# Kernel optimization log

Measured on AMD Instinct MI355X. Metric: run time of the kernel, lower is better.

## Reference

```python
import jax, jax.numpy as jnp
import numpy as np


def setup_inputs() -> dict:
    key = jax.random.key(0)
    k1, k2, k3 = jax.random.split(key, 3)
    B, C, S, D = 8, 256, 2048, 64
    a = jax.random.normal(k1, (B, C, S), dtype=jnp.float32)
    b = jax.random.normal(k2, (B, S, D), dtype=jnp.float32)
    c = jax.random.normal(k3, (B, S, D), dtype=jnp.float32)
    return {"a": a, "b": b, "c": c}


def reference(a, b, c):
    # mid[b, n, m] = softmax_m(b @ c^T), unscaled
    scores = jnp.einsum("bnd,bmd->bnm", b, c)
    mid = jax.nn.softmax(scores, axis=-1)  # [B, S, S]
    # out = a @ mid^T + a  -> [B, C, S]
    out = jnp.einsum("bcm,bnm->bcn", a, mid) + a
    return out
```

## Files before the change

kernel.cpp:

```cpp
#include <hip/hip_runtime.h>
#include <stdint.h>

#define S 2048
#define DHEAD 64
#define CDIM 256
#define NBATCH 8
#define NMT 16
#define NSTEP 32

typedef __attribute__((ext_vector_type(4))) float f32x4;
typedef __attribute__((ext_vector_type(8))) short s16x8;
typedef __attribute__((ext_vector_type(8))) _Float16 f16x8;
typedef __attribute__((ext_vector_type(4))) unsigned short u16x4;

static __device__ __forceinline__ unsigned short f2bf(float f) {
    unsigned int u = __builtin_bit_cast(unsigned int, f);
    unsigned int r = (u + 0x7FFFu + ((u >> 16) & 1u)) >> 16;
    return (unsigned short)r;
}
static __device__ __forceinline__ unsigned short f2h(float f) {
    _Float16 h = (_Float16)f;
    return __builtin_bit_cast(unsigned short, h);
}
static __device__ __forceinline__ float bf2f(unsigned short u) {
    return __builtin_bit_cast(float, (unsigned int)u << 16);
}

#define GLOAD16(g, l)                                                              \
    __builtin_amdgcn_global_load_lds(                                              \
        (const __attribute__((address_space(1))) void*)(g),                        \
        (__attribute__((address_space(3))) void*)(l), 16, 0, 0)

__global__ __launch_bounds__(256) void cvt_kernel(
    const float* __restrict__ a, const float* __restrict__ b, const float* __restrict__ c,
    unsigned short* __restrict__ a16, unsigned short* __restrict__ b16,
    unsigned short* __restrict__ c16)
{
    const int na4 = NBATCH * CDIM * S / 4;
    const int nbc4 = NBATCH * S * DHEAD / 4;
    int i0 = blockIdx.x * 256 + threadIdx.x;
    int stride = gridDim.x * 256;
    for (int i = i0; i < na4; i += stride) {
        f32x4 v = ((const f32x4*)a)[i];
        u16x4 o; o.x = f2bf(v.x); o.y = f2bf(v.y); o.z = f2bf(v.z); o.w = f2bf(v.w);
        ((u16x4*)a16)[i] = o;
    }
    for (int i = i0; i < nbc4; i += stride) {
        f32x4 v = ((const f32x4*)b)[i];
        u16x4 o; o.x = f2h(v.x); o.y = f2h(v.y); o.z = f2h(v.z); o.w = f2h(v.w);
        ((u16x4*)b16)[i] = o;
        f32x4 u = ((const f32x4*)c)[i];
        u16x4 p; p.x = f2h(u.x); p.y = f2h(u.y); p.z = f2h(u.z); p.w = f2h(u.w);
        ((u16x4*)c16)[i] = p;
    }
}

__global__ __launch_bounds__(256) void scores_kernel(
    const unsigned short* __restrict__ B16, const unsigned short* __restrict__ C16,
    unsigned short* __restrict__ E, float* __restrict__ Lp, int b0, int nb)
{
    const int bid = blockIdx.x;
    int lb, idx;
    if (nb == 8) { lb = bid & 7; idx = bid >> 3; }
    else { lb = bid / (NMT * 16); idx = bid - lb * (NMT * 16); }
    const int gb = b0 + lb;
    const int mt = idx & 15;
    const int m0 = mt * 128;
    const int n0 = (idx >> 4) * 128;
    const unsigned short* __restrict__ bp = B16 + (size_t)gb * S * DHEAD;
    const unsigned short* __restrict__ cp = C16 + (size_t)gb * S * DHEAD;
    unsigned short* __restrict__ Ep = E + (size_t)lb * S * S;

    extern __shared__ char smem[];
    unsigned short* cs = (unsigned short*)smem;
    unsigned short* bs = cs + 128 * 64;
    unsigned short* es = (unsigned short*)smem;
    float* Lsh = (float*)(smem + 34816);

    const int tid = threadIdx.x;
    const int lane = tid & 63;
    const int w = tid >> 6;
    const int wr = w >> 1, wc = w & 1;
    const int q = lane >> 4, r15 = lane & 15;

    #pragma unroll
    for (int t = 0; t < 4; ++t) {
        int r = w + 4 * t;
        int ch = r * 64 + lane;
        int row = ch >> 3;
        int off = ((ch & 7) ^ (row & 7)) * 8;
        GLOAD16(cp + (size_t)(m0 + row) * DHEAD + off, &cs[r * 512]);
        GLOAD16(bp + (size_t)(n0 + row) * DHEAD + off, &bs[r * 512]);
    }
    __syncthreads();

    f32x4 acc[4][4] = {};
    #pragma unroll
    for (int kk = 0; kk < 2; ++kk) {
        const int sz = ((kk * 4 + q) ^ (r15 & 7)) * 8;
        f16x8 af[4], bf[4];
        #pragma unroll
        for (int i = 0; i < 4; ++i)
            af[i] = *(const f16x8*)&cs[(wr * 64 + i * 16 + r15) * 64 + sz];
        #pragma unroll
        for (int j = 0; j < 4; ++j)
            bf[j] = *(const f16x8*)&bs[(wc * 64 + j * 16 + r15) * 64 + sz];
        #pragma unroll
        for (int i = 0; i < 4; ++i)
            #pragma unroll
            for (int j = 0; j < 4; ++j)
                acc[i][j] = __builtin_amdgcn_mfma_f32_16x16x32_f16(af[i], bf[j], acc[i][j], 0, 0, 0);
    }

    u16x4 pk[4][4];
    float sj[4] = {0.f, 0.f, 0.f, 0.f};
    #pragma unroll
    for (int i = 0; i < 4; ++i) {
        #pragma unroll
        for (int j = 0; j < 4; ++j) {
            float e0 = __expf(acc[i][j][0]);
            float e1 = __expf(acc[i][j][1]);
            float e2 = __expf(acc[i][j][2]);
            float e3 = __expf(acc[i][j][3]);
            pk[i][j].x = f2bf(e0); pk[i][j].y = f2bf(e1);
            pk[i][j].z = f2bf(e2); pk[i][j].w = f2bf(e3);
            sj[j] += (e0 + e1) + (e2 + e3);
        }
    }
    #pragma unroll
    for (int j = 0; j < 4; ++j) {
        sj[j] += __shfl_xor(sj[j], 16);
        sj[j] += __shfl_xor(sj[j], 32);
    }

    __syncthreads();

    #pragma unroll
    for (int i = 0; i < 4; ++i)
        #pragma unroll
        for (int j = 0; j < 4; ++j) {
            int nl = wc * 64 + j * 16 + r15;
            int ml = wr * 64 + i * 16 + q * 4;
            *(u16x4*)&es[nl * 136 + ml] = pk[i][j];
        }
    if (q == 0) {
        #pragma unroll
        for (int j = 0; j < 4; ++j)
            Lsh[wr * 128 + wc * 64 + j * 16 + r15] = sj[j];
    }
    __syncthreads();

    if (tid < 128)
        Lp[(size_t)lb * NMT * S + (size_t)mt * S + n0 + tid] = Lsh[tid] + Lsh[128 + tid];

    #pragma unroll
    for (int t = 0; t < 8; ++t) {
        int ch = tid + 256 * t;
        int row = ch >> 4, off = ch & 15;
        f32x4 v = *(const f32x4*)&es[row * 136 + off * 8];
        *(f32x4*)&Ep[(size_t)(n0 + row) * S + m0 + off * 8] = v;
    }
}

#define GEMM_DECODE()                                                             \
    const int tid = threadIdx.x;                                                  \
    const int lane = tid & 63;                                                    \
    const int w = tid >> 6;                                                       \
    const int wr = w >> 1, wc = w & 1;                                            \
    const int q = lane >> 4, r15 = lane & 15;                                     \
    int aRow[4], aOff[4], aR_[4], bRow[2], bOff[2], bR_[2];                       \
    _Pragma("unroll")                                                             \
    for (int t = 0; t < 4; ++t) {                                                 \
        int r = w + 4 * t, ch = r * 64 + lane;                                    \
        aR_[t] = r; aRow[t] = ch >> 3;                                            \
        aOff[t] = ((ch & 7) ^ ((ch >> 3) & 7)) * 8;                               \
    }                                                                             \
    _Pragma("unroll")                                                             \
    for (int t = 0; t < 2; ++t) {                                                 \
        int r = w + 4 * t, ch = r * 64 + lane;                                    \
        bR_[t] = r; bRow[t] = ch >> 3;                                            \
        bOff[t] = ((ch & 7) ^ ((ch >> 3) & 7)) * 8;                               \
    }

#define STAGEP(bufA, bufB, k0)                                                    \
    {                                                                             \
        _Pragma("unroll")                                                         \
        for (int t = 0; t < 4; ++t)                                               \
            GLOAD16(Ap + (size_t)(c0 + aRow[t]) * S + (k0) + aOff[t],             \
                    (bufA) + aR_[t] * 512);                                       \
        _Pragma("unroll")                                                         \
        for (int t = 0; t < 2; ++t)                                               \
            GLOAD16(Bp + (size_t)(n0 + bRow[t]) * S + (k0) + bOff[t],             \
                    (bufB) + bR_[t] * 512);                                       \
    }

#define GEMM_EPILOGUE()                                                           \
    float rcpL[2];                                                                \
    _Pragma("unroll")                                                             \
    for (int j = 0; j < 2; ++j) {                                                 \
        int n = n0 + wc * 32 + j * 16 + r15;                                      \
        float s = 0.f;                                                            \
        _Pragma("unroll")                                                         \
        for (int mt = 0; mt < NMT; ++mt)                                          \
            s += Lp[(size_t)lb * NMT * S + (size_t)mt * S + n];                   \
        rcpL[j] = 1.0f / s;                                                       \
    }                                                                             \
    _Pragma("unroll")                                                             \
    for (int i = 0; i < 4; ++i) {                                                 \
        _Pragma("unroll")                                                         \
        for (int rr = 0; rr < 4; ++rr) {                                          \
            int cc = c0 + wr * 64 + i * 16 + q * 4 + rr;                          \
            size_t base = (size_t)cc * S;                                         \
            _Pragma("unroll")                                                     \
            for (int j = 0; j < 2; ++j) {                                         \
                int n = n0 + wc * 32 + j * 16 + r15;                              \
                op[base + n] = acc[i][j][rr] * rcpL[j] + bf2f(Ap[base + n]);      \
            }                                                                     \
        }                                                                         \
    }

__global__ __launch_bounds__(256, 2) void gemm_kernel3(
    const unsigned short* __restrict__ a16, const unsigned short* __restrict__ E,
    const float* __restrict__ Lp, float* __restrict__ out, int b0, int nb)
{
    const int bid = blockIdx.x;
    int lb, idx;
    if (nb == 8) { lb = bid & 7; idx = bid >> 3; }
    else { lb = bid / 64; idx = bid - lb * 64; }
    const int gb = b0 + lb;
    const int nt = idx >> 1, ct = idx & 1;
    const int n0 = nt * 64, c0 = ct * 128;

    const unsigned short* __restrict__ Ap = a16 + (size_t)gb * CDIM * S;
    const unsigned short* __restrict__ Bp = E + (size_t)lb * S * S;
    float* __restrict__ op = out + (size_t)gb * CDIM * S;

    extern __shared__ char gsm[];
    unsigned short* As[3];
    unsigned short* Bs[3];
    #pragma unroll
    for (int u = 0; u < 3; ++u) {
        As[u] = (unsigned short*)gsm + u * (128 * 64 + 64 * 64);
        Bs[u] = As[u] + 128 * 64;
    }

    GEMM_DECODE();

    f32x4 acc[4][2] = {};

    STAGEP(As[0], Bs[0], 0);
    STAGEP(As[1], Bs[1], 64);

    const int sw0 = (q ^ (r15 & 7)) * 8;
    const int sw1 = ((4 + q) ^ (r15 & 7)) * 8;

    #pragma unroll
    for (int kt = 0; kt < NSTEP; ++kt) {
        const int cur = kt % 3;
        if (kt <= NSTEP - 3) {
            STAGEP(As[(kt + 2) % 3], Bs[(kt + 2) % 3], (kt + 2) * 64);
            asm volatile("s_waitcnt vmcnt(12)" ::: "memory");
        } else if (kt == NSTEP - 2) {
            asm volatile("s_waitcnt vmcnt(6)" ::: "memory");
        } else {
            asm volatile("s_waitcnt vmcnt(0)" ::: "memory");
        }
        __builtin_amdgcn_sched_barrier(0);
        __builtin_amdgcn_s_barrier();
        __builtin_amdgcn_sched_barrier(0);

        const unsigned short* Ar = As[cur];
        const unsigned short* Br = Bs[cur];
        #pragma unroll
        for (int kk = 0; kk < 2; ++kk) {
            const int sz = kk ? sw1 : sw0;
            s16x8 af[4], bf[2];
            #pragma unroll
            for (int i = 0; i < 4; ++i)
                af[i] = *(const s16x8*)&Ar[(wr * 64 + i * 16 + r15) * 64 + sz];
            #pragma unroll
            for (int j = 0; j < 2; ++j)
                bf[j] = *(const s16x8*)&Br[(wc * 32 + j * 16 + r15) * 64 + sz];
            __builtin_amdgcn_s_setprio(1);
            #pragma unroll
            for (int i = 0; i < 4; ++i)
                #pragma unroll
                for (int j = 0; j < 2; ++j)
                    acc[i][j] = __builtin_amdgcn_mfma_f32_16x16x32_bf16(af[i], bf[j], acc[i][j], 0, 0, 0);
            __builtin_amdgcn_s_setprio(0);
        }

        __builtin_amdgcn_sched_barrier(0);
        __builtin_amdgcn_s_barrier();
    }

    GEMM_EPILOGUE();
}

__global__ __launch_bounds__(256, 2) void gemm_kernel2(
    const unsigned short* __restrict__ a16, const unsigned short* __restrict__ E,
    const float* __restrict__ Lp, float* __restrict__ out, int b0, int nb)
{
    const int bid = blockIdx.x;
    int lb, idx;
    if (nb == 8) { lb = bid & 7; idx = bid >> 3; }
    else { lb = bid / 64; idx = bid - lb * 64; }
    const int gb = b0 + lb;
    const int nt = idx >> 1, ct = idx & 1;
    const int n0 = nt * 64, c0 = ct * 128;

    const unsigned short* __restrict__ Ap = a16 + (size_t)gb * CDIM * S;
    const unsigned short* __restrict__ Bp = E + (size_t)lb * S * S;
    float* __restrict__ op = out + (size_t)gb * CDIM * S;

    __shared__ unsigned short AsS[2][128 * 64];
    __shared__ unsigned short BsS[2][64 * 64];

    GEMM_DECODE();

    f32x4 acc[4][2] = {};

    STAGEP(AsS[0], BsS[0], 0);
    __syncthreads();

    const int sw0 = (q ^ (r15 & 7)) * 8;
    const int sw1 = ((4 + q) ^ (r15 & 7)) * 8;

    #pragma unroll 2
    for (int kt = 0; kt < NSTEP; ++kt) {
        const int cur = kt & 1;
        if (kt < NSTEP - 1) STAGEP(AsS[cur ^ 1], BsS[cur ^ 1], (kt + 1) * 64);

        #pragma unroll
        for (int kk = 0; kk < 2; ++kk) {
            const int sz = kk ? sw1 : sw0;
            s16x8 af[4], bf[2];
            #pragma unroll
            for (int i = 0; i < 4; ++i)
                af[i] = *(const s16x8*)&AsS[cur][(wr * 64 + i * 16 + r15) * 64 + sz];
            #pragma unroll
            for (int j = 0; j < 2; ++j)
                bf[j] = *(const s16x8*)&BsS[cur][(wc * 32 + j * 16 + r15) * 64 + sz];
            #pragma unroll
            for (int i = 0; i < 4; ++i)
                #pragma unroll
                for (int j = 0; j < 2; ++j)
                    acc[i][j] = __builtin_amdgcn_mfma_f32_16x16x32_bf16(af[i], bf[j], acc[i][j], 0, 0, 0);
        }
        __syncthreads();
    }

    GEMM_EPILOGUE();
}

extern "C" void kernel_launch(void* const* d_in, const int* in_sizes, int n_in,
                              void* d_out, int out_size, void* d_ws, size_t ws_size,
                              hipStream_t stream) {
    const float* a = (const float*)d_in[0];
    const float* b = (const float*)d_in[1];
    const float* c = (const float*)d_in[2];
    float* out = (float*)d_out;

    const size_t a16_bytes = (size_t)NBATCH * CDIM * S * 2;
    const size_t bc_bytes = (size_t)NBATCH * S * DHEAD * 2;
    const size_t head = a16_bytes + 2 * bc_bytes;
    const size_t perb = (size_t)S * S * 2 + (size_t)NMT * S * 4;
    int G = 1;
    if (ws_size > head + perb) {
        size_t g = (ws_size - head) / perb;
        G = (g >= NBATCH) ? NBATCH : (int)g;
        if (G < 1) G = 1;
    }
    unsigned short* a16 = (unsigned short*)d_ws;
    unsigned short* b16 = (unsigned short*)((char*)d_ws + a16_bytes);
    unsigned short* c16 = (unsigned short*)((char*)d_ws + a16_bytes + bc_bytes);
    unsigned short* E = (unsigned short*)((char*)d_ws + head);
    float* Lp = (float*)((char*)d_ws + head + (size_t)G * S * S * 2);

    const int gemm_lds3 = 3 * (128 * 64 + 64 * 64) * 2;
    hipError_t attr_ok = hipFuncSetAttribute(
        reinterpret_cast<const void*>(gemm_kernel3),
        hipFuncAttributeMaxDynamicSharedMemorySize, gemm_lds3);

    cvt_kernel<<<1024, 256, 0, stream>>>(a, b, c, a16, b16, c16);

    const size_t lds1 = 34816 + 2 * 128 * 4;
    for (int b0 = 0; b0 < NBATCH; b0 += G) {
        int nb = (NBATCH - b0 < G) ? (NBATCH - b0) : G;
        scores_kernel<<<NMT * 16 * nb, 256, lds1, stream>>>(b16, c16, E, Lp, b0, nb);
        if (attr_ok == hipSuccess)
            gemm_kernel3<<<64 * nb, 256, gemm_lds3, stream>>>(a16, E, Lp, out, b0, nb);
        else
            gemm_kernel2<<<64 * nb, 256, 0, stream>>>(a16, E, Lp, out, b0, nb);
    }
}
```

Before: 50.62 us.

## Make scores kernel loop over m-tiles with double-buffered C loads

```diff
diff --git a/kernel.cpp b/kernel.cpp
--- a/kernel.cpp
+++ b/kernel.cpp
@@ -5,8 +5,8 @@
 #define DHEAD 64
 #define CDIM 256
 #define NBATCH 8
-#define NMT 16
 #define NSTEP 32
+#define SMT 8
 
 typedef __attribute__((ext_vector_type(4))) float f32x4;
 typedef __attribute__((ext_vector_type(8))) short s16x8;
@@ -55,27 +55,27 @@
     }
 }
 
-__global__ __launch_bounds__(256) void scores_kernel(
+__global__ __launch_bounds__(256, 2) void scores_kernel(
     const unsigned short* __restrict__ B16, const unsigned short* __restrict__ C16,
     unsigned short* __restrict__ E, float* __restrict__ Lp, int b0, int nb)
 {
     const int bid = blockIdx.x;
     int lb, idx;
     if (nb == 8) { lb = bid & 7; idx = bid >> 3; }
-    else { lb = bid / (NMT * 16); idx = bid - lb * (NMT * 16); }
+    else { lb = bid / 64; idx = bid - lb * 64; }
     const int gb = b0 + lb;
-    const int mt = idx & 15;
-    const int m0 = mt * 128;
-    const int n0 = (idx >> 4) * 128;
+    const int nt = idx >> 1, mh = idx & 1;
+    const int n0 = nt * 64;
+    const int mbase = mh * (SMT * 128);
+
     const unsigned short* __restrict__ bp = B16 + (size_t)gb * S * DHEAD;
     const unsigned short* __restrict__ cp = C16 + (size_t)gb * S * DHEAD;
     unsigned short* __restrict__ Ep = E + (size_t)lb * S * S;
 
-    extern __shared__ char smem[];
-    unsigned short* cs = (unsigned short*)smem;
-    unsigned short* bs = cs + 128 * 64;
-    unsigned short* es = (unsigned short*)smem;
-    float* Lsh = (float*)(smem + 34816);
+    __shared__ unsigned short bs[64 * 64];
+    __shared__ unsigned short cs[2][128 * 64];
+    __shared__ unsigned short es[64 * 136];
+    __shared__ float Lsh[4 * 32];
 
     const int tid = threadIdx.x;
     const int lane = tid & 63;
@@ -83,82 +83,118 @@
     const int wr = w >> 1, wc = w & 1;
     const int q = lane >> 4, r15 = lane & 15;
 
+    int cRow[4], cOff[4], cR_[4], bRow[2], bOff[2], bR_[2];
     #pragma unroll
     for (int t = 0; t < 4; ++t) {
-        int r = w + 4 * t;
-        int ch = r * 64 + lane;
-        int row = ch >> 3;
-        int off = ((ch & 7) ^ (row & 7)) * 8;
-        GLOAD16(cp + (size_t)(m0 + row) * DHEAD + off, &cs[r * 512]);
-        GLOAD16(bp + (size_t)(n0 + row) * DHEAD + off, &bs[r * 512]);
-    }
-    __syncthreads();
-
-    f32x4 acc[4][4] = {};
-    #pragma unroll
-    for (int kk = 0; kk < 2; ++kk) {
-        const int sz = ((kk * 4 + q) ^ (r15 & 7)) * 8;
-        f16x8 af[4], bf[4];
+        int r = w + 4 * t, ch = r * 64 + lane;
+        cR_[t] = r; cRow[t] = ch >> 3;
+        cOff[t] = ((ch & 7) ^ ((ch >> 3) & 7)) * 8;
+    }
+    #pragma unroll
+    for (int t = 0; t < 2; ++t) {
+        int r = w + 4 * t, ch = r * 64 + lane;
+        bR_[t] = r; bRow[t] = ch >> 3;
+        bOff[t] = ((ch & 7) ^ ((ch >> 3) & 7)) * 8;
+    }
+
+#define SSTAGE_C(buf, m0)                                                          \
+    {                                                                              \
+        _Pragma("unroll")                                                          \
+        for (int t = 0; t < 4; ++t)                                                \
+            GLOAD16(cp + (size_t)((m0) + cRow[t]) * DHEAD + cOff[t],               \
+                    &cs[buf][cR_[t] * 512]);                                       \
+    }
+
+    #pragma unroll
+    for (int t = 0; t < 2; ++t)
+        GLOAD16(bp + (size_t)(n0 + bRow[t]) * DHEAD + bOff[t], &bs[bR_[t] * 512]);
+    SSTAGE_C(0, mbase);
+
+    float sj[2] = {0.f, 0.f};
+
+    #pragma unroll
+    for (int mt = 0; mt < SMT; ++mt) {
+        const int cur = mt & 1;
+        const int m0 = mbase + mt * 128;
+        if (mt < SMT - 1) {
+            SSTAGE_C(cur ^ 1, m0 + 128);
+            asm volatile("s_waitcnt vmcnt(4)" ::: "memory");
+        } else {
+            asm volatile("s_waitcnt vmcnt(0)" ::: "memory");
+        }
+        __builtin_amdgcn_sched_barrier(0);
+        __builtin_amdgcn_s_barrier();
+        __builtin_amdgcn_sched_barrier(0);
+
+        f32x4 acc[4][2] = {};
+        #pragma unroll
+        for (int kk = 0; kk < 2; ++kk) {
+            const int sz = ((kk * 4 + q) ^ (r15 & 7)) * 8;
+            f16x8 af[4], bf[2];
+            #pragma unroll
+            for (int i = 0; i < 4; ++i)
+                af[i] = *(const f16x8*)&cs[cur][(wr * 64 + i * 16 + r15) * 64 + sz];
+            #pragma unroll
+            for (int j = 0; j < 2; ++j)
+                bf[j] = *(const f16x8*)&bs[(wc * 32 + j * 16 + r15) * 64 + sz];
+            __builtin_amdgcn_s_setprio(1);
+            #pragma unroll
+            for (int i = 0; i < 4; ++i)
+                #pragma unroll
+                for (int j = 0; j < 2; ++j)
+                    acc[i][j] = __builtin_amdgcn_mfma_f32_16x16x32_f16(af[i], bf[j], acc[i][j], 0, 0, 0);
+            __builtin_amdgcn_s_setprio(0);
+        }
+
+        u16x4 pk[4][2];
         #pragma unroll
         for (int i = 0; i < 4; ++i)
-            af[i] = *(const f16x8*)&cs[(wr * 64 + i * 16 + r15) * 64 + sz];
-        #pragma unroll
-        for (int j = 0; j < 4; ++j)
-            bf[j] = *(const f16x8*)&bs[(wc * 64 + j * 16 + r15) * 64 + sz];
+            #pragma unroll
+            for (int j = 0; j < 2; ++j) {
+                float e0 = __expf(acc[i][j][0]);
+                float e1 = __expf(acc[i][j][1]);
+                float e2 = __expf(acc[i][j][2]);
+                float e3 = __expf(acc[i][j][3]);
+                sj[j] += (e0 + e1) + (e2 + e3);
+                pk[i][j].x = f2bf(e0); pk[i][j].y = f2bf(e1);
+                pk[i][j].z = f2bf(e2); pk[i][j].w = f2bf(e3);
+            }
+
+        __syncthreads();
         #pragma unroll
         for (int i = 0; i < 4; ++i)
             #pragma unroll
-            for (int j = 0; j < 4; ++j)
-                acc[i][j] = __builtin_amdgcn_mfma_f32_16x16x32_f16(af[i], bf[j], acc[i][j], 0, 0, 0);
-    }
-
-    u16x4 pk[4][4];
-    float sj[4] = {0.f, 0.f, 0.f, 0.f};
-    #pragma unroll
-    for (int i = 0; i < 4; ++i) {
-        #pragma unroll
-        for (int j = 0; j < 4; ++j) {
-            float e0 = __expf(acc[i][j][0]);
-            float e1 = __expf(acc[i][j][1]);
-            float e2 = __expf(acc[i][j][2]);
-            float e3 = __expf(acc[i][j][3]);
-            pk[i][j].x = f2bf(e0); pk[i][j].y = f2bf(e1);
-            pk[i][j].z = f2bf(e2); pk[i][j].w = f2bf(e3);
-            sj[j] += (e0 + e1) + (e2 + e3);
-        }
-    }
-    #pragma unroll
-    for (int j = 0; j < 4; ++j) {
+            for (int j = 0; j < 2; ++j) {
+                int nl = wc * 32 + j * 16 + r15;
+                int ml = wr * 64 + i * 16 + q * 4;
+                *(u16x4*)&es[nl * 136 + ml] = pk[i][j];
+            }
+        __syncthreads();
+
+        #pragma unroll
+        for (int t = 0; t < 4; ++t) {
+            int ch = tid + 256 * t;
+            int row = ch >> 4, off = ch & 15;
+            f32x4 v = *(const f32x4*)&es[row * 136 + off * 8];
+            *(f32x4*)&Ep[(size_t)(n0 + row) * S + m0 + off * 8] = v;
+        }
+    }
+#undef SSTAGE_C
+
+    #pragma unroll
+    for (int j = 0; j < 2; ++j) {
         sj[j] += __shfl_xor(sj[j], 16);
         sj[j] += __shfl_xor(sj[j], 32);
     }
-
+    if (lane < 16) {
+        Lsh[w * 32 + r15] = sj[0];
+        Lsh[w * 32 + 16 + r15] = sj[1];
+    }
     __syncthreads();
-
-    #pragma unroll
-    for (int i = 0; i < 4; ++i)
-        #pragma unroll
-        for (int j = 0; j < 4; ++j) {
-            int nl = wc * 64 + j * 16 + r15;
-            int ml = wr * 64 + i * 16 + q * 4;
-            *(u16x4*)&es[nl * 136 + ml] = pk[i][j];
-        }
-    if (q == 0) {
-        #pragma unroll
-        for (int j = 0; j < 4; ++j)
-            Lsh[wr * 128 + wc * 64 + j * 16 + r15] = sj[j];
-    }
-    __syncthreads();
-
-    if (tid < 128)
-        Lp[(size_t)lb * NMT * S + (size_t)mt * S + n0 + tid] = Lsh[tid] + Lsh[128 + tid];
-
-    #pragma unroll
-    for (int t = 0; t < 8; ++t) {
-        int ch = tid + 256 * t;
-        int row = ch >> 4, off = ch & 15;
-        f32x4 v = *(const f32x4*)&es[row * 136 + off * 8];
-        *(f32x4*)&Ep[(size_t)(n0 + row) * S + m0 + off * 8] = v;
+    if (tid < 64) {
+        int wcn = tid >> 5, rem = tid & 31;
+        float s = Lsh[wcn * 32 + rem] + Lsh[(2 + wcn) * 32 + rem];
+        Lp[((size_t)lb * 2 + mh) * S + n0 + tid] = s;
     }
 }
 
@@ -199,10 +235,7 @@
     _Pragma("unroll")                                                             \
     for (int j = 0; j < 2; ++j) {                                                 \
         int n = n0 + wc * 32 + j * 16 + r15;                                      \
-        float s = 0.f;                                                            \
-        _Pragma("unroll")                                                         \
-        for (int mt = 0; mt < NMT; ++mt)                                          \
-            s += Lp[(size_t)lb * NMT * S + (size_t)mt * S + n];                   \
+        float s = Lp[(size_t)lb * 2 * S + n] + Lp[((size_t)lb * 2 + 1) * S + n]; \
         rcpL[j] = 1.0f / s;                                                       \
     }                                                                             \
     _Pragma("unroll")                                                             \
@@ -364,7 +397,7 @@
     const size_t a16_bytes = (size_t)NBATCH * CDIM * S * 2;
     const size_t bc_bytes = (size_t)NBATCH * S * DHEAD * 2;
     const size_t head = a16_bytes + 2 * bc_bytes;
-    const size_t perb = (size_t)S * S * 2 + (size_t)NMT * S * 4;
+    const size_t perb = (size_t)S * S * 2 + (size_t)2 * S * 4;
     int G = 1;
     if (ws_size > head + perb) {
         size_t g = (ws_size - head) / perb;
@@ -384,10 +417,9 @@
 
     cvt_kernel<<<1024, 256, 0, stream>>>(a, b, c, a16, b16, c16);
 
-    const size_t lds1 = 34816 + 2 * 128 * 4;
     for (int b0 = 0; b0 < NBATCH; b0 += G) {
         int nb = (NBATCH - b0 < G) ? (NBATCH - b0) : G;
-        scores_kernel<<<NMT * 16 * nb, 256, lds1, stream>>>(b16, c16, E, Lp, b0, nb);
+        scores_kernel<<<64 * nb, 256, 0, stream>>>(b16, c16, E, Lp, b0, nb);
         if (attr_ok == hipSuccess)
             gemm_kernel3<<<64 * nb, 256, gemm_lds3, stream>>>(a16, E, Lp, out, b0, nb);
         else
```

Result: no change. 50.68 us (+0.1%).
